# Optimization experiments

Measured on AMD Instinct MI355X. Metric: run time of the kernel, lower is better.

Reference implementation:

```python
import jax, jax.numpy as jnp
import numpy as np

TEMP = 0.5  # temperature_f from init


def setup_inputs() -> dict:
    key = jax.random.key(0)
    k1, k2, k3 = jax.random.split(key, 3)
    B, d = 4096, 128
    h_i = jax.random.normal(k1, (B, d), dtype=jnp.float32)
    h_j = jax.random.normal(k2, (B, d), dtype=jnp.float32)
    S = jax.random.uniform(k3, (B, B), dtype=jnp.float32)
    return {"h_i": h_i, "h_j": h_j, "S": S}


def reference(h_i, h_j, S):
    B = h_i.shape[0]
    N = 2 * B
    h = jnp.concatenate([h_i, h_j], axis=0)                 # [N, d]
    sim = jnp.matmul(h, h.T) / TEMP                          # [N, N]
    # S_2 = 1 - (S**2).repeat(2,2); sim1 = sim * S_2
    S2 = 1.0 - jnp.tile(S * S, (2, 2))                       # [N, N]
    sim1 = sim * S2
    # positives: diag(sim, +B) and diag(sim, -B)
    idx = jnp.arange(B)
    pos = jnp.concatenate([sim[idx, idx + B], sim[idx + B, idx]])  # [N]
    # negatives mask: exclude diagonal and the positive-pair positions
    i = jnp.arange(N)[:, None]
    j = jnp.arange(N)[None, :]
    neg_mask = ~((i == j) | (j == (i + B) % N))              # [N, N], N-2 True per row
    neg = jnp.where(neg_mask, sim1, -jnp.inf)                # masked entries drop out of logsumexp
    # CrossEntropy(label=0, reduction='sum') over logits=[pos, negatives]:
    # loss_n = logsumexp(logits_n) - pos_n  (order of negatives is irrelevant)
    logits = jnp.concatenate([pos[:, None], neg], axis=1)    # [N, N-1] effective
    lse = jax.nn.logsumexp(logits, axis=1)
    loss = jnp.sum(lse - pos) / N
    return loss
```

## Files before the change

kernel.cpp:

```cpp
#include <hip/hip_runtime.h>
#include <hip/hip_bf16.h>

#define B_ROWS 4096
#define NN     8192
#define DD     128
#define NSPLIT 64
#define NTRI   2080
#define SPA    68
#define CSHIFT 128.0f

typedef __attribute__((ext_vector_type(8))) short s8v;
typedef __attribute__((ext_vector_type(4))) float f4v;
typedef __attribute__((ext_vector_type(2))) float f2v;
typedef __attribute__((ext_vector_type(4))) unsigned short u16x4;
typedef unsigned int u32;

static constexpr float SCALE_H = 1.6986436f;
static constexpr float SCALE2  = 2.8853900818f;
static constexpr float LN2     = 0.6931471805599453f;

__device__ __forceinline__ float fast_exp2(float x) {
#if __has_builtin(__builtin_amdgcn_exp2f)
    return __builtin_amdgcn_exp2f(x);
#else
    return exp2f(x);
#endif
}

__device__ __forceinline__ unsigned short s2m_pack(float x, bool msk) {
    float s2 = msk ? 0.f : 1.f - x * x;
    union { __hip_bfloat16 h; unsigned short u; } cv;
    cv.h = __float2bfloat16(s2);
    return cv.u;
}

__device__ __forceinline__ float bf16f(unsigned short u) {
    return __uint_as_float(((u32)u) << 16);
}

typedef __attribute__((address_space(1))) const u32 gu32;
typedef __attribute__((address_space(3))) u32 lu32;
__device__ __forceinline__ void gload_lds16(const void* g, void* l) {
    __builtin_amdgcn_global_load_lds((gu32*)g, (lu32*)l, 16, 0, 0);
}

__global__ void hpos_kernel(const float* __restrict__ hi, const float* __restrict__ hj,
                            __hip_bfloat16* __restrict__ hb, float* __restrict__ pos2) {
    int w = threadIdx.x >> 6, l = threadIdx.x & 63;
    int row = blockIdx.x * 4 + w;
    f2v a = ((const f2v*)(hi + (size_t)row * DD))[l];
    f2v b = ((const f2v*)(hj + (size_t)row * DD))[l];
    float d = a[0] * b[0] + a[1] * b[1];
    #pragma unroll
    for (int off = 32; off; off >>= 1) d += __shfl_xor(d, off, 64);
    if (l == 0) pos2[row] = SCALE2 * d;
    union { ushort2 u2; __hip_bfloat16 h[2]; } ua, ub;
    ua.h[0] = __float2bfloat16(a[0] * SCALE_H);
    ua.h[1] = __float2bfloat16(a[1] * SCALE_H);
    ub.h[0] = __float2bfloat16(b[0] * SCALE_H);
    ub.h[1] = __float2bfloat16(b[1] * SCALE_H);
    ((ushort2*)(hb + (size_t)row * DD))[l] = ua.u2;
    ((ushort2*)(hb + (size_t)(row + B_ROWS) * DD))[l] = ub.u2;
}

__global__ __launch_bounds__(512, 2)
void main_kernel(const __hip_bfloat16* __restrict__ hb, const float* __restrict__ S,
                 float* __restrict__ ssplit) {
    __shared__ short ldsB[128][128];
    __shared__ float sAf[64 * 64];
    __shared__ unsigned short sB[64][SPA];
    __shared__ float mrg[768];

    const int orig = blockIdx.x;
    const int bid  = (orig & 7) * (NTRI / 8) + (orig >> 3);
    int j = (int)((sqrtf(8.0f * (float)bid + 1.0f) - 1.0f) * 0.5f);
    while (((j + 1) * (j + 2)) / 2 <= bid) ++j;
    while ((j * (j + 1)) / 2 > bid) --j;
    const int i = bid - (j * (j + 1)) / 2;
    const bool diag = (i == j);

    const int tid = threadIdx.x;
    const int l  = tid & 63;
    const int w  = tid >> 6;
    const int wm = w >> 1, wn = w & 1;
    const int lc = l & 15;
    const int lk = l >> 4;
    const int r64 = i * 64, c64 = j * 64;

    const s8v* hb8 = (const s8v*)hb;

    #pragma unroll
    for (int i2 = 0; i2 < 4; i2++) {
        const int rowb = w * 16 + i2 * 4;
        const int lrw  = rowb + lk;
        const int grow = c64 + ((lrw < 64) ? lrw : (lrw - 64 + B_ROWS));
        const int sc16 = lc ^ (lrw & 7);
        gload_lds16((const char*)hb + ((size_t)grow << 8) + (sc16 << 4),
                    (char*)&ldsB[rowb][0]);
    }

    #pragma unroll
    for (int i2 = 0; i2 < 2; i2++) {
        const int seg  = w * 2 + i2;
        const int rowp = seg * 4 + lk;
        gload_lds16((const char*)(S + (size_t)(r64 + rowp) * B_ROWS + c64) + (lc << 4),
                    (char*)&sAf[seg * 4 * 64]);
    }

    {
        const int rr = tid >> 3;
        const int c8 = (tid & 7) * 8;
        const float* gB = S + (size_t)(c64 + rr) * B_ROWS + r64 + c8;
        f4v b0 = ((const f4v*)gB)[0], b1 = ((const f4v*)gB)[1];
        u16x4 pb0, pb1;
        #pragma unroll
        for (int e = 0; e < 4; e++) {
            pb0[e] = s2m_pack(b0[e], false);
            pb1[e] = s2m_pack(b1[e], false);
        }
        *(u16x4*)&sB[rr][c8]     = pb0;
        *(u16x4*)&sB[rr][c8 + 4] = pb1;
    }

    s8v afr[2][4];
    #pragma unroll
    for (int fm = 0; fm < 2; fm++) {
        int ar = (r64 + wm * 16 + lc) + fm * B_ROWS;
        #pragma unroll
        for (int kk = 0; kk < 4; kk++)
            afr[fm][kk] = hb8[ar * 16 + kk * 4 + lk];
    }
    __syncthreads();

    const char* bp[4];
    {
        const char* bb = (const char*)ldsB + (wn * 32 + lc) * 256;
        #pragma unroll
        for (int kk = 0; kk < 4; kk++)
            bp[kk] = bb + (((kk * 4 + lk) ^ (lc & 7)) << 4);
    }
    f4v acc[2][2][2];
    #pragma unroll
    for (int fm = 0; fm < 2; fm++)
        #pragma unroll
        for (int fh = 0; fh < 2; fh++)
            #pragma unroll
            for (int cg = 0; cg < 2; cg++) acc[fm][fh][cg] = f4v{0.f, 0.f, 0.f, 0.f};
    #pragma unroll
    for (int kk = 0; kk < 4; kk++) {
        #pragma unroll
        for (int fh = 0; fh < 2; fh++)
            #pragma unroll
            for (int cg = 0; cg < 2; cg++) {
                s8v bf = *(const s8v*)(bp[kk] + fh * 16384 + cg * 4096);
                acc[0][fh][cg] = __builtin_amdgcn_mfma_f32_16x16x32_bf16(
                    afr[0][kk], bf, acc[0][fh][cg], 0, 0, 0);
                acc[1][fh][cg] = __builtin_amdgcn_mfma_f32_16x16x32_bf16(
                    afr[1][kk], bf, acc[1][fh][cg], 0, 0, 0);
            }
    }

    float rsum[2][4], csum[2][2];
    #pragma unroll
    for (int fm = 0; fm < 2; fm++)
        #pragma unroll
        for (int r = 0; r < 4; r++) rsum[fm][r] = 0.f;
    csum[0][0] = csum[0][1] = csum[1][0] = csum[1][1] = 0.f;

    #pragma unroll
    for (int r = 0; r < 4; r++) {
        const int rr = wm * 16 + lk * 4 + r;
        #pragma unroll
        for (int cg = 0; cg < 2; cg++) {
            const int cc = wn * 32 + cg * 16 + lc;
            const float Sv  = sAf[rr * 64 + cc];
            const float s2a = (diag && (cc == rr)) ? 0.f : fmaf(-Sv, Sv, 1.f);
            const float s2b = bf16f(sB[cc][rr]);
            #pragma unroll
            for (int fm = 0; fm < 2; fm++)
                #pragma unroll
                for (int fh = 0; fh < 2; fh++) {
                    const float a = acc[fm][fh][cg][r];
                    rsum[fm][r]  += fast_exp2(fmaf(a, s2a, -CSHIFT));
                    csum[fh][cg] += fast_exp2(fmaf(a, s2b, -CSHIFT));
                }
        }
    }

    #pragma unroll
    for (int fm = 0; fm < 2; fm++) {
        #pragma unroll
        for (int r = 0; r < 4; r++) {
            float ss = rsum[fm][r];
            #pragma unroll
            for (int off = 1; off < 16; off <<= 1) ss += __shfl_xor(ss, off, 64);
            if (lc == 0) mrg[wn * 128 + fm * 64 + (wm * 16 + lk * 4 + r)] = ss;
        }
    }
    #pragma unroll
    for (int fh = 0; fh < 2; fh++) {
        #pragma unroll
        for (int cg = 0; cg < 2; cg++) {
            float ss = csum[fh][cg];
            ss += __shfl_xor(ss, 16, 64);
            ss += __shfl_xor(ss, 32, 64);
            if (l < 16) mrg[256 + wm * 128 + fh * 64 + (wn * 32 + cg * 16 + lc)] = ss;
        }
    }
    __syncthreads();

    if (tid < 128) {
        int fm = tid >> 6, rho = tid & 63;
        float v = mrg[fm * 64 + rho] + mrg[128 + fm * 64 + rho];
        ssplit[(size_t)j * NN + (r64 + rho + fm * B_ROWS)] = v;
    } else if (!diag && tid < 256) {
        int t2 = tid - 128, fh = t2 >> 6, cc = t2 & 63;
        float v = mrg[256 +   0 + fh * 64 + cc] + mrg[256 + 128 + fh * 64 + cc]
                + mrg[256 + 256 + fh * 64 + cc] + mrg[256 + 384 + fh * 64 + cc];
        ssplit[(size_t)i * NN + (c64 + cc + fh * B_ROWS)] = v;
    }
}

__global__ __launch_bounds__(256)
void reduce_kernel(const float* __restrict__ ssplit, const float* __restrict__ pos2,
                   float* __restrict__ partial) {
    __shared__ float red[256];
    const int r = threadIdx.x & 31;
    const int s = threadIdx.x >> 5;
    const int n = blockIdx.x * 32 + r;
    float ssum = 0.f;
    #pragma unroll
    for (int k = 0; k < 8; k++)
        ssum += ssplit[(size_t)(s + 8 * k) * NN + n];
    red[threadIdx.x] = ssum;
    __syncthreads();
    if (threadIdx.x < 32) {
        float t = 0.f;
        #pragma unroll
        for (int k = 0; k < 8; k++) t += red[threadIdx.x + 32 * k];
        float p = pos2[n & (B_ROWS - 1)];
        float Ssum = t + fast_exp2(p - CSHIFT);
        red[threadIdx.x] = (CSHIFT + log2f(Ssum)) - p;
    }
    __syncthreads();
    if (threadIdx.x == 0) {
        float acc = 0.f;
        #pragma unroll
        for (int k = 0; k < 32; k++) acc += red[k];
        partial[blockIdx.x] = acc;
    }
}

__global__ __launch_bounds__(256)
void final_kernel(const float* __restrict__ partial, float* __restrict__ out) {
    __shared__ float red[256];
    red[threadIdx.x] = partial[threadIdx.x];
    __syncthreads();
    for (int st = 128; st; st >>= 1) {
        if (threadIdx.x < st) red[threadIdx.x] += red[threadIdx.x + st];
        __syncthreads();
    }
    if (threadIdx.x == 0) out[0] = red[0] * (LN2 / (float)NN);
}

extern "C" void kernel_launch(void* const* d_in, const int* in_sizes, int n_in,
                              void* d_out, int out_size, void* d_ws, size_t ws_size,
                              hipStream_t stream) {
    (void)in_sizes; (void)n_in; (void)out_size; (void)ws_size;
    const float* hi = (const float*)d_in[0];
    const float* hj = (const float*)d_in[1];
    const float* S  = (const float*)d_in[2];

    char* ws = (char*)d_ws;
    __hip_bfloat16* hb = (__hip_bfloat16*)ws;
    float* pos2   = (float*)(ws + 2097152);
    float* ssplit = (float*)(ws + 2097152 + 16384);
    float* partial= (float*)(ws + 2097152 + 16384 + 2097152);

    hpos_kernel<<<1024, 256, 0, stream>>>(hi, hj, hb, pos2);
    main_kernel<<<NTRI, 512, 0, stream>>>(hb, S, ssplit);
    reduce_kernel<<<256, 256, 0, stream>>>(ssplit, pos2, partial);
    final_kernel<<<1, 256, 0, stream>>>(partial, (float*)d_out);
}
```

Before: 45.18 us.

## Load S tiles directly into registers and drop LDS staging buffers

The S tile and its transpose are now read straight from global memory into registers per thread, instead of being staged through LDS. This removes the sAf and sB shared arrays and the bf16 packing step. The smaller LDS footprint lets launch bounds ask for four blocks per CU instead of two. In exchange, the transposed loads are strided, poorly coalesced global reads, and the loads are issued after the barrier, so their latency overlaps less with other work.

```diff
diff --git a/kernel.cpp b/kernel.cpp
--- a/kernel.cpp
+++ b/kernel.cpp
@@ -6,13 +6,11 @@
 #define DD     128
 #define NSPLIT 64
 #define NTRI   2080
-#define SPA    68
 #define CSHIFT 128.0f
 
 typedef __attribute__((ext_vector_type(8))) short s8v;
 typedef __attribute__((ext_vector_type(4))) float f4v;
 typedef __attribute__((ext_vector_type(2))) float f2v;
-typedef __attribute__((ext_vector_type(4))) unsigned short u16x4;
 typedef unsigned int u32;
 
 static constexpr float SCALE_H = 1.6986436f;
@@ -25,17 +23,6 @@
 #else
     return exp2f(x);
 #endif
-}
-
-__device__ __forceinline__ unsigned short s2m_pack(float x, bool msk) {
-    float s2 = msk ? 0.f : 1.f - x * x;
-    union { __hip_bfloat16 h; unsigned short u; } cv;
-    cv.h = __float2bfloat16(s2);
-    return cv.u;
-}
-
-__device__ __forceinline__ float bf16f(unsigned short u) {
-    return __uint_as_float(((u32)u) << 16);
 }
 
 typedef __attribute__((address_space(1))) const u32 gu32;
@@ -63,12 +50,10 @@
     ((ushort2*)(hb + (size_t)(row + B_ROWS) * DD))[l] = ub.u2;
 }
 
-__global__ __launch_bounds__(512, 2)
+__global__ __launch_bounds__(512, 4)
 void main_kernel(const __hip_bfloat16* __restrict__ hb, const float* __restrict__ S,
                  float* __restrict__ ssplit) {
     __shared__ short ldsB[128][128];
-    __shared__ float sAf[64 * 64];
-    __shared__ unsigned short sB[64][SPA];
     __shared__ float mrg[768];
 
     const int orig = blockIdx.x;
@@ -99,29 +84,6 @@
                     (char*)&ldsB[rowb][0]);
     }
 
-    #pragma unroll
-    for (int i2 = 0; i2 < 2; i2++) {
-        const int seg  = w * 2 + i2;
-        const int rowp = seg * 4 + lk;
-        gload_lds16((const char*)(S + (size_t)(r64 + rowp) * B_ROWS + c64) + (lc << 4),
-                    (char*)&sAf[seg * 4 * 64]);
-    }
-
-    {
-        const int rr = tid >> 3;
-        const int c8 = (tid & 7) * 8;
-        const float* gB = S + (size_t)(c64 + rr) * B_ROWS + r64 + c8;
-        f4v b0 = ((const f4v*)gB)[0], b1 = ((const f4v*)gB)[1];
-        u16x4 pb0, pb1;
-        #pragma unroll
-        for (int e = 0; e < 4; e++) {
-            pb0[e] = s2m_pack(b0[e], false);
-            pb1[e] = s2m_pack(b1[e], false);
-        }
-        *(u16x4*)&sB[rr][c8]     = pb0;
-        *(u16x4*)&sB[rr][c8 + 4] = pb1;
-    }
-
     s8v afr[2][4];
     #pragma unroll
     for (int fm = 0; fm < 2; fm++) {
@@ -131,6 +93,21 @@
             afr[fm][kk] = hb8[ar * 16 + kk * 4 + lk];
     }
     __syncthreads();
+
+    float sva[4][2], svb[4][2];
+    {
+        const float* gSr = S + (size_t)(r64 + wm * 16 + lk * 4) * B_ROWS
+                             + (c64 + wn * 32 + lc);
+        const float* gSc = S + (size_t)(c64 + wn * 32 + lc) * B_ROWS
+                             + (r64 + wm * 16 + lk * 4);
+        #pragma unroll
+        for (int r = 0; r < 4; r++)
+            #pragma unroll
+            for (int cg = 0; cg < 2; cg++) {
+                sva[r][cg] = gSr[(size_t)r * B_ROWS + cg * 16];
+                svb[r][cg] = gSc[(size_t)(cg * 16) * B_ROWS + r];
+            }
+    }
 
     const char* bp[4];
     {
@@ -173,9 +150,10 @@
         #pragma unroll
         for (int cg = 0; cg < 2; cg++) {
             const int cc = wn * 32 + cg * 16 + lc;
-            const float Sv  = sAf[rr * 64 + cc];
+            const float Sv  = sva[r][cg];
             const float s2a = (diag && (cc == rr)) ? 0.f : fmaf(-Sv, Sv, 1.f);
-            const float s2b = bf16f(sB[cc][rr]);
+            const float Sw  = svb[r][cg];
+            const float s2b = fmaf(-Sw, Sw, 1.f);
             #pragma unroll
             for (int fm = 0; fm < 2; fm++)
                 #pragma unroll
```

Measured after the change: 48.37 us. 1.07x slower.
